# Performance work log

Measured on AMD Instinct MI355X. Metric: run time of the kernel, lower is better.

Reference implementation:

```python
import jax, jax.numpy as jnp
import numpy as np

B, H = 8192, 768


def _mk_linear(key, fan_in, fan_out):
    k1, k2 = jax.random.split(key)
    lim = 1.0 / np.sqrt(fan_in)
    W = jax.random.uniform(k1, (fan_out, fan_in), jnp.float32, -lim, lim)
    b = jax.random.uniform(k2, (fan_out,), jnp.float32, -lim, lim)
    return W, b


def setup_inputs() -> dict:
    key = jax.random.key(0)
    ks = jax.random.split(key, 6)
    modal_a = jax.random.normal(ks[0], (B, H), jnp.float32)
    modal_b = jax.random.normal(ks[1], (B, H), jnp.float32)
    W1m, b1m = _mk_linear(ks[2], H, H)
    W2m, b2m = _mk_linear(ks[3], H, H)
    W1v, b1v = _mk_linear(ks[4], H, H)
    W2v, b2v = _mk_linear(ks[5], H, H)
    return {"modal_a": modal_a, "modal_b": modal_b,
            "W1m": W1m, "b1m": b1m, "W2m": W2m, "b2m": b2m,
            "W1v": W1v, "b1v": b1v, "W2v": W2v, "b2v": b2v}


def reference(modal_a, modal_b, W1m, b1m, W2m, b2m, W1v, b1v, W2v, b2v):
    # mlp_mu: Linear -> Tanh -> Linear
    mu = jnp.tanh(modal_a @ W1m.T + b1m) @ W2m.T + b2m              # [B,H]
    # mlp_logvar: Linear -> Tanh -> Linear -> Tanh
    logvar = jnp.tanh(jnp.tanh(modal_a @ W1v.T + b1v) @ W2v.T + b2v)  # [B,H]
    inv_var = jnp.exp(-logvar)

    positive = -(mu - modal_b) ** 2 * 0.5 * inv_var                  # [B,H]

    # mean_j (mu[j] - mu[i])^2 = E[mu^2] - 2*mu[i]*E[mu] + mu[i]^2  (per feature dim)
    # Algebraic reduction of the O(B^2*H) tile in the original code.
    mu_mean = jnp.mean(mu, axis=0)                                   # [H]
    mu_sq_mean = jnp.mean(mu * mu, axis=0)                           # [H]
    pair_sq = mu_sq_mean - 2.0 * mu * mu_mean + mu * mu              # [B,H]
    negative = -pair_sq * 0.5 * inv_var                              # [B,H]

    pos_sum = jnp.sum(positive, axis=-1)                             # [B]
    neg_sum = jnp.sum(negative, axis=-1)                             # [B]
    lld = jnp.mean(pos_sum)
    bound = jnp.mean(pos_sum - neg_sum)
    return (lld, bound)
```

## Files before the change

### kernel.cpp

```cpp
#include <hip/hip_runtime.h>
#include <math.h>

typedef float v16f __attribute__((ext_vector_type(16)));
typedef short bf16x8 __attribute__((ext_vector_type(8)));

#define AS1 __attribute__((address_space(1)))
#define AS3 __attribute__((address_space(3)))

static constexpr int Bn = 8192;
static constexpr int Hn = 768;
static constexpr float invB = 1.0f / 8192.0f;

__device__ __forceinline__ short f32_to_bf16(float x) {
    union { float f; unsigned u; } v; v.f = x;
    unsigned r = (v.u + 0x7FFFu + ((v.u >> 16) & 1u)) >> 16;
    return (short)r;
}

__device__ __forceinline__ float fast_tanh(float x) {
    float xc = fminf(fmaxf(x, -15.0f), 15.0f);
    float e = __expf(2.0f * xc);
    float r = __builtin_amdgcn_rcpf(e + 1.0f);
    return 1.0f - 2.0f * r;
}

__global__ void prep_kernel(const float* __restrict__ A,
                            const float* __restrict__ W1m, const float* __restrict__ W2m,
                            const float* __restrict__ W1v, const float* __restrict__ W2v,
                            short* __restrict__ A_bf,
                            short* __restrict__ W1m_bf, short* __restrict__ W2m_bf,
                            short* __restrict__ W1v_bf, short* __restrict__ W2v_bf,
                            float* __restrict__ zbuf, int nzero) {
    const int tid = blockIdx.x * blockDim.x + threadIdx.x;
    if (tid < nzero) zbuf[tid] = 0.0f;
    constexpr int A4 = Bn * Hn / 4;
    constexpr int W4 = Hn * Hn / 4;
    const int total = A4 + 4 * W4;
    const int stride = gridDim.x * blockDim.x;
    for (int i = tid; i < total; i += stride) {
        const float* s; short* d; int j;
        if (i < A4) { s = A; d = A_bf; j = i; }
        else {
            int k = i - A4; int w = k / W4; j = k - w * W4;
            s = (w == 0) ? W1m : (w == 1) ? W2m : (w == 2) ? W1v : W2v;
            d = (w == 0) ? W1m_bf : (w == 1) ? W2m_bf : (w == 2) ? W1v_bf : W2v_bf;
        }
        float4 v = ((const float4*)s)[j];
        short4 o;
        o.x = f32_to_bf16(v.x); o.y = f32_to_bf16(v.y);
        o.z = f32_to_bf16(v.z); o.w = f32_to_bf16(v.w);
        ((short4*)d)[j] = o;
    }
}

__launch_bounds__(256, 3)
__global__ void gemm_l1(const short* __restrict__ A_g,
                        const short* __restrict__ Wm_g, const short* __restrict__ Wv_g,
                        const float* __restrict__ bm, const float* __restrict__ bv,
                        short* __restrict__ outm, short* __restrict__ outv) {
    constexpr int K = Hn;
    __shared__ __align__(16) short As[128 * 64];
    __shared__ __align__(16) short Ws[128 * 64];

    const int z = blockIdx.z;
    const short* W = z ? Wv_g : Wm_g;
    const float* bias = z ? bv : bm;
    short* out = z ? outv : outm;

    const int t = threadIdx.x;
    const int row0 = blockIdx.x * 128;
    const int col0 = blockIdx.y * 128;
    const int w = t >> 6, lane = t & 63;
    const int wm = w >> 1, wn = w & 1;
    const int lc = lane & 31, lh = lane >> 5;

    const int rt = t >> 3;
    const int bsrc = (t & 7) ^ (rt & 7);

    const short* pA[4]; const short* pW[4];
#pragma unroll
    for (int i = 0; i < 4; ++i) {
        pA[i] = A_g + (size_t)(row0 + i * 32 + rt) * K + bsrc * 8;
        pW[i] = W + (size_t)(col0 + i * 32 + rt) * K + bsrc * 8;
    }

    v16f acc[2][2] = {};

    for (int k0 = 0; k0 < K; k0 += 64) {
#pragma unroll
        for (int i = 0; i < 4; ++i) {
            __builtin_amdgcn_global_load_lds((AS1 void*)pA[i], (AS3 void*)&As[i * 2048 + t * 8], 16, 0, 0);
            __builtin_amdgcn_global_load_lds((AS1 void*)pW[i], (AS3 void*)&Ws[i * 2048 + t * 8], 16, 0, 0);
            pA[i] += 64; pW[i] += 64;
        }
        __syncthreads();
#pragma unroll
        for (int ks = 0; ks < 4; ++ks) {
            const int kb = ks * 2 + lh;
            bf16x8 af[2], bfr[2];
#pragma unroll
            for (int mt = 0; mt < 2; ++mt) {
                int m = wm * 64 + mt * 32 + lc;
                af[mt] = *(const bf16x8*)&As[m * 64 + ((kb ^ (m & 7)) << 3)];
            }
#pragma unroll
            for (int nt = 0; nt < 2; ++nt) {
                int n = wn * 64 + nt * 32 + lc;
                bfr[nt] = *(const bf16x8*)&Ws[n * 64 + ((kb ^ (n & 7)) << 3)];
            }
#pragma unroll
            for (int mt = 0; mt < 2; ++mt)
#pragma unroll
                for (int nt = 0; nt < 2; ++nt)
                    acc[mt][nt] = __builtin_amdgcn_mfma_f32_32x32x16_bf16(af[mt], bfr[nt], acc[mt][nt], 0, 0, 0);
        }
        __syncthreads();
    }

#pragma unroll
    for (int nt = 0; nt < 2; ++nt) {
        const int col = col0 + wn * 64 + nt * 32 + lc;
        const float bc = bias[col];
#pragma unroll
        for (int mt = 0; mt < 2; ++mt) {
#pragma unroll
            for (int reg = 0; reg < 16; ++reg) {
                const int row = row0 + wm * 64 + mt * 32 + (reg & 3) + 8 * (reg >> 2) + 4 * lh;
                out[(size_t)row * Hn + col] = f32_to_bf16(fast_tanh(acc[mt][nt][reg] + bc));
            }
        }
    }
}

__launch_bounds__(256, 2)
__global__ void gemm_l2(const short* __restrict__ Am_g, const short* __restrict__ Av_g,
                        const short* __restrict__ Wm_g, const short* __restrict__ Wv_g,
                        const float* __restrict__ bm, const float* __restrict__ bv,
                        const float* __restrict__ mb,
                        float* __restrict__ cs, float* __restrict__ cs2,
                        float* __restrict__ siv, float* __restrict__ sivmu,
                        float* __restrict__ accum) {
    constexpr int K = Hn;
    __shared__ __align__(16) short As_m[128 * 64];
    __shared__ __align__(16) short As_v[128 * 64];
    __shared__ __align__(16) short Ws_m[128 * 64];
    __shared__ __align__(16) short Ws_v[128 * 64];

    const int t = threadIdx.x;
    const int row0 = blockIdx.x * 128;
    const int col0 = blockIdx.y * 128;
    const int w = t >> 6, lane = t & 63;
    const int wm = w >> 1, wn = w & 1;
    const int lc = lane & 31, lh = lane >> 5;

    const int rt = t >> 3;
    const int bsrc = (t & 7) ^ (rt & 7);

    const short* pAm[4]; const short* pAv[4]; const short* pWm[4]; const short* pWv[4];
#pragma unroll
    for (int i = 0; i < 4; ++i) {
        pAm[i] = Am_g + (size_t)(row0 + i * 32 + rt) * K + bsrc * 8;
        pAv[i] = Av_g + (size_t)(row0 + i * 32 + rt) * K + bsrc * 8;
        pWm[i] = Wm_g + (size_t)(col0 + i * 32 + rt) * K + bsrc * 8;
        pWv[i] = Wv_g + (size_t)(col0 + i * 32 + rt) * K + bsrc * 8;
    }

    v16f accm[2][2] = {}, accv[2][2] = {};

    for (int k0 = 0; k0 < K; k0 += 64) {
#pragma unroll
        for (int i = 0; i < 4; ++i) {
            __builtin_amdgcn_global_load_lds((AS1 void*)pAm[i], (AS3 void*)&As_m[i * 2048 + t * 8], 16, 0, 0);
            __builtin_amdgcn_global_load_lds((AS1 void*)pAv[i], (AS3 void*)&As_v[i * 2048 + t * 8], 16, 0, 0);
            __builtin_amdgcn_global_load_lds((AS1 void*)pWm[i], (AS3 void*)&Ws_m[i * 2048 + t * 8], 16, 0, 0);
            __builtin_amdgcn_global_load_lds((AS1 void*)pWv[i], (AS3 void*)&Ws_v[i * 2048 + t * 8], 16, 0, 0);
            pAm[i] += 64; pAv[i] += 64; pWm[i] += 64; pWv[i] += 64;
        }
        __syncthreads();
#pragma unroll
        for (int ks = 0; ks < 4; ++ks) {
            const int kb = ks * 2 + lh;
            bf16x8 am[2], av[2], bmf[2], bvf[2];
#pragma unroll
            for (int mt = 0; mt < 2; ++mt) {
                int m = wm * 64 + mt * 32 + lc;
                int off = m * 64 + ((kb ^ (m & 7)) << 3);
                am[mt] = *(const bf16x8*)&As_m[off];
                av[mt] = *(const bf16x8*)&As_v[off];
            }
#pragma unroll
            for (int nt = 0; nt < 2; ++nt) {
                int n = wn * 64 + nt * 32 + lc;
                int off = n * 64 + ((kb ^ (n & 7)) << 3);
                bmf[nt] = *(const bf16x8*)&Ws_m[off];
                bvf[nt] = *(const bf16x8*)&Ws_v[off];
            }
#pragma unroll
            for (int mt = 0; mt < 2; ++mt)
#pragma unroll
                for (int nt = 0; nt < 2; ++nt) {
                    accm[mt][nt] = __builtin_amdgcn_mfma_f32_32x32x16_bf16(am[mt], bmf[nt], accm[mt][nt], 0, 0, 0);
                    accv[mt][nt] = __builtin_amdgcn_mfma_f32_32x32x16_bf16(av[mt], bvf[nt], accv[mt][nt], 0, 0, 0);
                }
        }
        __syncthreads();
    }

    float pos = 0.f, q = 0.f;
#pragma unroll
    for (int nt = 0; nt < 2; ++nt) {
        const int col = col0 + wn * 64 + nt * 32 + lc;
        const float bmc = bm[col], bvc = bv[col];
        float c1 = 0.f, c2 = 0.f, c3 = 0.f, c4 = 0.f;
#pragma unroll
        for (int mt = 0; mt < 2; ++mt) {
#pragma unroll
            for (int reg = 0; reg < 16; ++reg) {
                const int row = row0 + wm * 64 + mt * 32 + (reg & 3) + 8 * (reg >> 2) + 4 * lh;
                float mu = accm[mt][nt][reg] + bmc;
                float tv = fast_tanh(accv[mt][nt][reg] + bvc);
                float iv = __expf(-tv);
                float mbv = mb[(size_t)row * Hn + col];
                float d = mu - mbv;
                pos += iv * d * d;
                q   += iv * mu * mu;
                c1 += mu; c2 += mu * mu; c3 += iv; c4 += iv * mu;
            }
        }
        c1 += __shfl_xor(c1, 32); c2 += __shfl_xor(c2, 32);
        c3 += __shfl_xor(c3, 32); c4 += __shfl_xor(c4, 32);
        if (lh == 0) {
            atomicAdd(&cs[col], c1);
            atomicAdd(&cs2[col], c2);
            atomicAdd(&siv[col], c3);
            atomicAdd(&sivmu[col], c4);
        }
    }
    for (int off = 32; off > 0; off >>= 1) {
        pos += __shfl_down(pos, off);
        q   += __shfl_down(q, off);
    }
    __shared__ float redP[4], redQ[4];
    if (lane == 0) { redP[w] = pos; redQ[w] = q; }
    __syncthreads();
    if (t == 0) {
        atomicAdd(&accum[0], redP[0] + redP[1] + redP[2] + redP[3]);
        atomicAdd(&accum[1], redQ[0] + redQ[1] + redQ[2] + redQ[3]);
    }
}

__global__ void combine_kernel(const float* __restrict__ cs, const float* __restrict__ cs2,
                               const float* __restrict__ siv, const float* __restrict__ sivmu,
                               const float* __restrict__ accum, float* __restrict__ out) {
    const int h = threadIdx.x;
    float term = siv[h] * cs2[h] - 2.0f * sivmu[h] * cs[h];
    for (int off = 32; off > 0; off >>= 1) term += __shfl_down(term, off);
    __shared__ float red[12];
    const int lane = h & 63, w = h >> 6;
    if (lane == 0) red[w] = term;
    __syncthreads();
    if (h == 0) {
        float T = 0.f;
#pragma unroll
        for (int i = 0; i < 12; ++i) T += red[i];
        float P = accum[0];
        float Q = accum[1];
        float pos_sum = -0.5f * P;
        float neg_sum = -0.5f * (T * invB + Q);
        out[0] = pos_sum * invB;
        out[1] = (pos_sum - neg_sum) * invB;
    }
}

extern "C" void kernel_launch(void* const* d_in, const int* in_sizes, int n_in,
                              void* d_out, int out_size, void* d_ws, size_t ws_size,
                              hipStream_t stream) {
    const float* modal_a = (const float*)d_in[0];
    const float* modal_b = (const float*)d_in[1];
    const float* W1m = (const float*)d_in[2];
    const float* b1m = (const float*)d_in[3];
    const float* W2m = (const float*)d_in[4];
    const float* b2m = (const float*)d_in[5];
    const float* W1v = (const float*)d_in[6];
    const float* b1v = (const float*)d_in[7];
    const float* W2v = (const float*)d_in[8];
    const float* b2v = (const float*)d_in[9];
    float* out = (float*)d_out;

    char* ws = (char*)d_ws;
    constexpr size_t szAH = (size_t)Bn * Hn * 2;
    constexpr size_t szW  = (size_t)Hn * Hn * 2;
    short* A_bf   = (short*)(ws);
    short* h1m    = (short*)(ws + szAH);
    short* h1v    = (short*)(ws + 2 * szAH);
    short* W1m_bf = (short*)(ws + 3 * szAH);
    short* W2m_bf = (short*)(ws + 3 * szAH + szW);
    short* W1v_bf = (short*)(ws + 3 * szAH + 2 * szW);
    short* W2v_bf = (short*)(ws + 3 * szAH + 3 * szW);
    float* cs     = (float*)(ws + 3 * szAH + 4 * szW);
    float* cs2    = cs + Hn;
    float* siv    = cs + 2 * Hn;
    float* sivmu  = cs + 3 * Hn;
    float* accum  = cs + 4 * Hn;

    prep_kernel<<<1280, 256, 0, stream>>>(modal_a, W1m, W2m, W1v, W2v,
                                          A_bf, W1m_bf, W2m_bf, W1v_bf, W2v_bf,
                                          cs, 4 * Hn + 2);

    gemm_l1<<<dim3(Bn / 128, Hn / 128, 2), 256, 0, stream>>>(
        A_bf, W1m_bf, W1v_bf, b1m, b1v, h1m, h1v);

    gemm_l2<<<dim3(Bn / 128, Hn / 128), 256, 0, stream>>>(
        h1m, h1v, W2m_bf, W2v_bf, b2m, b2v, modal_b,
        cs, cs2, siv, sivmu, accum);

    combine_kernel<<<1, 768, 0, stream>>>(cs, cs2, siv, sivmu, accum, out);
}
```

Baseline: 180.8 us.

## Switch to 16x16 MFMA, stage L1 stores via LDS, narrow L2 tiles, fuse combine

Both GEMMs move from 32x32x16 to 16x16x32 bf16 MFMA tiles. The layer-1 epilogue is staged through shared memory so each row is written to global memory as 16-byte vectors instead of scattered 2-byte stores. Layer 2 halves its N tile to 64 and raises occupancy to 3 blocks per CU. The separate combine kernel is removed by having the last-finishing block, detected with an atomic counter, compute the final result, which saves a launch but adds a threadfence and a serialized tail in one block.

```diff
diff --git a/kernel.cpp b/kernel.cpp
--- a/kernel.cpp
+++ b/kernel.cpp
@@ -1,7 +1,7 @@
 #include <hip/hip_runtime.h>
 #include <math.h>
 
-typedef float v16f __attribute__((ext_vector_type(16)));
+typedef float v4f __attribute__((ext_vector_type(4)));
 typedef short bf16x8 __attribute__((ext_vector_type(8)));
 
 #define AS1 __attribute__((address_space(1)))
@@ -59,8 +59,9 @@
                         const float* __restrict__ bm, const float* __restrict__ bv,
                         short* __restrict__ outm, short* __restrict__ outv) {
     constexpr int K = Hn;
-    __shared__ __align__(16) short As[128 * 64];
-    __shared__ __align__(16) short Ws[128 * 64];
+    __shared__ __align__(16) short smem[16384];
+    short* As = smem;
+    short* Ws = smem + 8192;
 
     const int z = blockIdx.z;
     const short* W = z ? Wv_g : Wm_g;
@@ -72,7 +73,7 @@
     const int col0 = blockIdx.y * 128;
     const int w = t >> 6, lane = t & 63;
     const int wm = w >> 1, wn = w & 1;
-    const int lc = lane & 31, lh = lane >> 5;
+    const int lr = lane & 15, quad = lane >> 4;
 
     const int rt = t >> 3;
     const int bsrc = (t & 7) ^ (rt & 7);
@@ -84,7 +85,7 @@
         pW[i] = W + (size_t)(col0 + i * 32 + rt) * K + bsrc * 8;
     }
 
-    v16f acc[2][2] = {};
+    v4f acc[4][4] = {};
 
     for (int k0 = 0; k0 < K; k0 += 64) {
 #pragma unroll
@@ -95,112 +96,127 @@
         }
         __syncthreads();
 #pragma unroll
-        for (int ks = 0; ks < 4; ++ks) {
-            const int kb = ks * 2 + lh;
-            bf16x8 af[2], bfr[2];
-#pragma unroll
-            for (int mt = 0; mt < 2; ++mt) {
-                int m = wm * 64 + mt * 32 + lc;
+        for (int s = 0; s < 2; ++s) {
+            const int kb = s * 4 + quad;
+            bf16x8 af[4], bfr[4];
+#pragma unroll
+            for (int mt = 0; mt < 4; ++mt) {
+                int m = wm * 64 + mt * 16 + lr;
                 af[mt] = *(const bf16x8*)&As[m * 64 + ((kb ^ (m & 7)) << 3)];
             }
 #pragma unroll
-            for (int nt = 0; nt < 2; ++nt) {
-                int n = wn * 64 + nt * 32 + lc;
+            for (int nt = 0; nt < 4; ++nt) {
+                int n = wn * 64 + nt * 16 + lr;
                 bfr[nt] = *(const bf16x8*)&Ws[n * 64 + ((kb ^ (n & 7)) << 3)];
             }
 #pragma unroll
-            for (int mt = 0; mt < 2; ++mt)
-#pragma unroll
-                for (int nt = 0; nt < 2; ++nt)
-                    acc[mt][nt] = __builtin_amdgcn_mfma_f32_32x32x16_bf16(af[mt], bfr[nt], acc[mt][nt], 0, 0, 0);
-        }
-        __syncthreads();
-    }
-
-#pragma unroll
-    for (int nt = 0; nt < 2; ++nt) {
-        const int col = col0 + wn * 64 + nt * 32 + lc;
-        const float bc = bias[col];
-#pragma unroll
-        for (int mt = 0; mt < 2; ++mt) {
-#pragma unroll
-            for (int reg = 0; reg < 16; ++reg) {
-                const int row = row0 + wm * 64 + mt * 32 + (reg & 3) + 8 * (reg >> 2) + 4 * lh;
-                out[(size_t)row * Hn + col] = f32_to_bf16(fast_tanh(acc[mt][nt][reg] + bc));
-            }
-        }
-    }
-}
-
-__launch_bounds__(256, 2)
+            for (int mt = 0; mt < 4; ++mt)
+#pragma unroll
+                for (int nt = 0; nt < 4; ++nt)
+                    acc[mt][nt] = __builtin_amdgcn_mfma_f32_16x16x32_bf16(af[mt], bfr[nt], acc[mt][nt], 0, 0, 0);
+        }
+        __syncthreads();
+    }
+
+#pragma unroll
+    for (int nt = 0; nt < 4; ++nt) {
+        const int col_l = wn * 64 + nt * 16 + lr;
+        const float bc = bias[col0 + col_l];
+#pragma unroll
+        for (int mt = 0; mt < 4; ++mt) {
+#pragma unroll
+            for (int r = 0; r < 4; ++r) {
+                const int row_l = wm * 64 + mt * 16 + quad * 4 + r;
+                smem[row_l * 128 + col_l] = f32_to_bf16(fast_tanh(acc[mt][nt][r] + bc));
+            }
+        }
+    }
+    __syncthreads();
+#pragma unroll
+    for (int p = 0; p < 8; ++p) {
+        const int row_l = p * 16 + (t >> 4);
+        const int seg = (t & 15) * 8;
+        bf16x8 v = *(const bf16x8*)&smem[row_l * 128 + seg];
+        *(bf16x8*)&out[(size_t)(row0 + row_l) * Hn + col0 + seg] = v;
+    }
+}
+
+__launch_bounds__(256, 3)
 __global__ void gemm_l2(const short* __restrict__ Am_g, const short* __restrict__ Av_g,
                         const short* __restrict__ Wm_g, const short* __restrict__ Wv_g,
                         const float* __restrict__ bm, const float* __restrict__ bv,
                         const float* __restrict__ mb,
                         float* __restrict__ cs, float* __restrict__ cs2,
                         float* __restrict__ siv, float* __restrict__ sivmu,
-                        float* __restrict__ accum) {
+                        float* __restrict__ accum, float* __restrict__ outp) {
     constexpr int K = Hn;
     __shared__ __align__(16) short As_m[128 * 64];
     __shared__ __align__(16) short As_v[128 * 64];
-    __shared__ __align__(16) short Ws_m[128 * 64];
-    __shared__ __align__(16) short Ws_v[128 * 64];
+    __shared__ __align__(16) short Ws_m[64 * 64];
+    __shared__ __align__(16) short Ws_v[64 * 64];
 
     const int t = threadIdx.x;
     const int row0 = blockIdx.x * 128;
-    const int col0 = blockIdx.y * 128;
+    const int col0 = blockIdx.y * 64;
     const int w = t >> 6, lane = t & 63;
     const int wm = w >> 1, wn = w & 1;
-    const int lc = lane & 31, lh = lane >> 5;
+    const int lr = lane & 15, quad = lane >> 4;
 
     const int rt = t >> 3;
     const int bsrc = (t & 7) ^ (rt & 7);
 
-    const short* pAm[4]; const short* pAv[4]; const short* pWm[4]; const short* pWv[4];
+    const short* pAm[4]; const short* pAv[4]; const short* pWm[2]; const short* pWv[2];
 #pragma unroll
     for (int i = 0; i < 4; ++i) {
         pAm[i] = Am_g + (size_t)(row0 + i * 32 + rt) * K + bsrc * 8;
         pAv[i] = Av_g + (size_t)(row0 + i * 32 + rt) * K + bsrc * 8;
+    }
+#pragma unroll
+    for (int i = 0; i < 2; ++i) {
         pWm[i] = Wm_g + (size_t)(col0 + i * 32 + rt) * K + bsrc * 8;
         pWv[i] = Wv_g + (size_t)(col0 + i * 32 + rt) * K + bsrc * 8;
     }
 
-    v16f accm[2][2] = {}, accv[2][2] = {};
+    v4f accm[4][2] = {}, accv[4][2] = {};
 
     for (int k0 = 0; k0 < K; k0 += 64) {
 #pragma unroll
         for (int i = 0; i < 4; ++i) {
             __builtin_amdgcn_global_load_lds((AS1 void*)pAm[i], (AS3 void*)&As_m[i * 2048 + t * 8], 16, 0, 0);
             __builtin_amdgcn_global_load_lds((AS1 void*)pAv[i], (AS3 void*)&As_v[i * 2048 + t * 8], 16, 0, 0);
+            pAm[i] += 64; pAv[i] += 64;
+        }
+#pragma unroll
+        for (int i = 0; i < 2; ++i) {
             __builtin_amdgcn_global_load_lds((AS1 void*)pWm[i], (AS3 void*)&Ws_m[i * 2048 + t * 8], 16, 0, 0);
             __builtin_amdgcn_global_load_lds((AS1 void*)pWv[i], (AS3 void*)&Ws_v[i * 2048 + t * 8], 16, 0, 0);
-            pAm[i] += 64; pAv[i] += 64; pWm[i] += 64; pWv[i] += 64;
-        }
-        __syncthreads();
-#pragma unroll
-        for (int ks = 0; ks < 4; ++ks) {
-            const int kb = ks * 2 + lh;
-            bf16x8 am[2], av[2], bmf[2], bvf[2];
-#pragma unroll
-            for (int mt = 0; mt < 2; ++mt) {
-                int m = wm * 64 + mt * 32 + lc;
+            pWm[i] += 64; pWv[i] += 64;
+        }
+        __syncthreads();
+#pragma unroll
+        for (int s = 0; s < 2; ++s) {
+            const int kb = s * 4 + quad;
+            bf16x8 am[4], av[4], bmf[2], bvf[2];
+#pragma unroll
+            for (int mt = 0; mt < 4; ++mt) {
+                int m = wm * 64 + mt * 16 + lr;
                 int off = m * 64 + ((kb ^ (m & 7)) << 3);
                 am[mt] = *(const bf16x8*)&As_m[off];
                 av[mt] = *(const bf16x8*)&As_v[off];
             }
 #pragma unroll
             for (int nt = 0; nt < 2; ++nt) {
-                int n = wn * 64 + nt * 32 + lc;
+                int n = wn * 32 + nt * 16 + lr;
                 int off = n * 64 + ((kb ^ (n & 7)) << 3);
                 bmf[nt] = *(const bf16x8*)&Ws_m[off];
                 bvf[nt] = *(const bf16x8*)&Ws_v[off];
             }
 #pragma unroll
-            for (int mt = 0; mt < 2; ++mt)
+            for (int mt = 0; mt < 4; ++mt)
 #pragma unroll
                 for (int nt = 0; nt < 2; ++nt) {
-                    accm[mt][nt] = __builtin_amdgcn_mfma_f32_32x32x16_bf16(am[mt], bmf[nt], accm[mt][nt], 0, 0, 0);
-                    accv[mt][nt] = __builtin_amdgcn_mfma_f32_32x32x16_bf16(av[mt], bvf[nt], accv[mt][nt], 0, 0, 0);
+                    accm[mt][nt] = __builtin_amdgcn_mfma_f32_16x16x32_bf16(am[mt], bmf[nt], accm[mt][nt], 0, 0, 0);
+                    accv[mt][nt] = __builtin_amdgcn_mfma_f32_16x16x32_bf16(av[mt], bvf[nt], accv[mt][nt], 0, 0, 0);
                 }
         }
         __syncthreads();
@@ -209,16 +225,16 @@
     float pos = 0.f, q = 0.f;
 #pragma unroll
     for (int nt = 0; nt < 2; ++nt) {
-        const int col = col0 + wn * 64 + nt * 32 + lc;
+        const int col = col0 + wn * 32 + nt * 16 + lr;
         const float bmc = bm[col], bvc = bv[col];
         float c1 = 0.f, c2 = 0.f, c3 = 0.f, c4 = 0.f;
 #pragma unroll
-        for (int mt = 0; mt < 2; ++mt) {
-#pragma unroll
-            for (int reg = 0; reg < 16; ++reg) {
-                const int row = row0 + wm * 64 + mt * 32 + (reg & 3) + 8 * (reg >> 2) + 4 * lh;
-                float mu = accm[mt][nt][reg] + bmc;
-                float tv = fast_tanh(accv[mt][nt][reg] + bvc);
+        for (int mt = 0; mt < 4; ++mt) {
+#pragma unroll
+            for (int r = 0; r < 4; ++r) {
+                const int row = row0 + wm * 64 + mt * 16 + quad * 4 + r;
+                float mu = accm[mt][nt][r] + bmc;
+                float tv = fast_tanh(accv[mt][nt][r] + bvc);
                 float iv = __expf(-tv);
                 float mbv = mb[(size_t)row * Hn + col];
                 float d = mu - mbv;
@@ -227,9 +243,11 @@
                 c1 += mu; c2 += mu * mu; c3 += iv; c4 += iv * mu;
             }
         }
-        c1 += __shfl_xor(c1, 32); c2 += __shfl_xor(c2, 32);
-        c3 += __shfl_xor(c3, 32); c4 += __shfl_xor(c4, 32);
-        if (lh == 0) {
+        c1 += __shfl_xor(c1, 16); c1 += __shfl_xor(c1, 32);
+        c2 += __shfl_xor(c2, 16); c2 += __shfl_xor(c2, 32);
+        c3 += __shfl_xor(c3, 16); c3 += __shfl_xor(c3, 32);
+        c4 += __shfl_xor(c4, 16); c4 += __shfl_xor(c4, 32);
+        if (quad == 0) {
             atomicAdd(&cs[col], c1);
             atomicAdd(&cs2[col], c2);
             atomicAdd(&siv[col], c3);
@@ -243,32 +261,37 @@
     __shared__ float redP[4], redQ[4];
     if (lane == 0) { redP[w] = pos; redQ[w] = q; }
     __syncthreads();
+    __shared__ int is_last;
     if (t == 0) {
         atomicAdd(&accum[0], redP[0] + redP[1] + redP[2] + redP[3]);
         atomicAdd(&accum[1], redQ[0] + redQ[1] + redQ[2] + redQ[3]);
-    }
-}
-
-__global__ void combine_kernel(const float* __restrict__ cs, const float* __restrict__ cs2,
-                               const float* __restrict__ siv, const float* __restrict__ sivmu,
-                               const float* __restrict__ accum, float* __restrict__ out) {
-    const int h = threadIdx.x;
-    float term = siv[h] * cs2[h] - 2.0f * sivmu[h] * cs[h];
-    for (int off = 32; off > 0; off >>= 1) term += __shfl_down(term, off);
-    __shared__ float red[12];
-    const int lane = h & 63, w = h >> 6;
-    if (lane == 0) red[w] = term;
+        __threadfence();
+        unsigned old = atomicAdd((unsigned int*)&accum[3], 1u);
+        is_last = (old == gridDim.x * gridDim.y - 1) ? 1 : 0;
+    }
     __syncthreads();
-    if (h == 0) {
-        float T = 0.f;
-#pragma unroll
-        for (int i = 0; i < 12; ++i) T += red[i];
-        float P = accum[0];
-        float Q = accum[1];
-        float pos_sum = -0.5f * P;
-        float neg_sum = -0.5f * (T * invB + Q);
-        out[0] = pos_sum * invB;
-        out[1] = (pos_sum - neg_sum) * invB;
+    if (is_last) {
+        float term = 0.f;
+        for (int h = t; h < Hn; h += 256) {
+            float v1 = atomicAdd(&cs[h], 0.0f);
+            float v2 = atomicAdd(&cs2[h], 0.0f);
+            float v3 = atomicAdd(&siv[h], 0.0f);
+            float v4 = atomicAdd(&sivmu[h], 0.0f);
+            term += v3 * v2 - 2.0f * v4 * v1;
+        }
+        for (int off = 32; off > 0; off >>= 1) term += __shfl_down(term, off);
+        __shared__ float redT[4];
+        if (lane == 0) redT[w] = term;
+        __syncthreads();
+        if (t == 0) {
+            float T = redT[0] + redT[1] + redT[2] + redT[3];
+            float P = atomicAdd(&accum[0], 0.0f);
+            float Q = atomicAdd(&accum[1], 0.0f);
+            float pos_sum = -0.5f * P;
+            float neg_sum = -0.5f * (T * invB + Q);
+            outp[0] = pos_sum * invB;
+            outp[1] = (pos_sum - neg_sum) * invB;
+        }
     }
 }
 
@@ -305,14 +328,12 @@
 
     prep_kernel<<<1280, 256, 0, stream>>>(modal_a, W1m, W2m, W1v, W2v,
                                           A_bf, W1m_bf, W2m_bf, W1v_bf, W2v_bf,
-                                          cs, 4 * Hn + 2);
+                                          cs, 4 * Hn + 8);
 
     gemm_l1<<<dim3(Bn / 128, Hn / 128, 2), 256, 0, stream>>>(
         A_bf, W1m_bf, W1v_bf, b1m, b1v, h1m, h1v);
 
-    gemm_l2<<<dim3(Bn / 128, Hn / 128), 256, 0, stream>>>(
+    gemm_l2<<<dim3(Bn / 128, Hn / 64), 256, 0, stream>>>(
         h1m, h1v, W2m_bf, W2v_bf, b2m, b2v, modal_b,
-        cs, cs2, siv, sivmu, accum);
-
-    combine_kernel<<<1, 768, 0, stream>>>(cs, cs2, siv, sivmu, accum, out);
-}
+        cs, cs2, siv, sivmu, accum, out);
+}
```

New measurement: 181.9 us. About the same (+0.6%).
